# Kernel tuning notes

Measured on AMD Instinct MI355X. Metric: run time of the kernel, lower is better.

## Reference

```python
import jax, jax.numpy as jnp
import numpy as np

MAX_DISP = 48
N, C, H, W = 4, 32, 256, 512

def setup_inputs() -> dict:
    key = jax.random.key(0)
    k1, k2 = jax.random.split(key)
    l_fmap = jax.random.normal(k1, (N, C, H, W), dtype=jnp.float32)
    r_fmap = jax.random.normal(k2, (N, C, H, W), dtype=jnp.float32)
    return {"l_fmap": l_fmap, "r_fmap": r_fmap, "use_naive": 1}

def _cost_volume(l_fmap, r_fmap):
    # cost[n, d, h, w] = mean_c l[n,c,h,w] * r[n,c,h,w-d], zero where w < d
    n, c, h, w = l_fmap.shape
    items = []
    for d in range(MAX_DISP):
        if d == 0:
            r_shift = r_fmap
        else:
            # shift right by d with zero padding on the left (columns w<d -> 0)
            r_shift = jnp.pad(r_fmap[..., : w - d], ((0, 0), (0, 0), (0, 0), (d, 0)))
        items.append(jnp.mean(l_fmap * r_shift, axis=1))  # [n, h, w]
    return jnp.stack(items, axis=1)  # [n, max_disp, h, w]

def reference(l_fmap, r_fmap, use_naive):
    # naive and conv2d paths compute identical math; use_naive is ignored
    return _cost_volume(l_fmap, r_fmap)
```

## Files before the change

### kernel.cpp

```cpp
#include <hip/hip_runtime.h>

#define CC 32
#define HH 256
#define WW 512
#define NN 4
#define MAXD 48

#define WT 256
#define RW (WT + MAXD)
#define DTILE 8
#define WTILE 4
#define NT 384

__global__ __launch_bounds__(NT, 6)
void cost_volume_kernel(const float* __restrict__ L,
                        const float* __restrict__ R,
                        float* __restrict__ out)
{
    __shared__ float r_s[CC][RW];

    const int t  = threadIdx.x;
    const int w0 = blockIdx.x * WT;
    const int h  = blockIdx.y;
    const int n  = blockIdx.z;

    const size_t chw  = (size_t)HH * WW;
    const size_t rowB = (size_t)n * CC * chw + (size_t)h * WW;

    #pragma unroll
    for (int k = 0; k < 7; ++k) {
        int idx = t + NT * k;
        if (idx < 2432) {
            int c   = idx / 76;
            int j4  = idx - c * 76;
            int g   = w0 - MAXD + 4 * j4;
            float4 v = make_float4(0.f, 0.f, 0.f, 0.f);
            if (g >= 0)
                v = *(const float4*)(R + rowB + (size_t)c * chw + g);
            *(float4*)&r_s[c][4 * j4] = v;
        }
    }
    __syncthreads();

    const int wg = t & 63;
    const int dg = t >> 6;
    const int wb = wg * WTILE;
    const int d0 = dg * DTILE;
    const int jA = wb + 40 - d0;

    float acc[DTILE][WTILE];
    #pragma unroll
    for (int k = 0; k < DTILE; ++k)
        #pragma unroll
        for (int i = 0; i < WTILE; ++i)
            acc[k][i] = 0.f;

    const float* lp = L + rowB + w0 + wb;
    float4 lv0 = *(const float4*)(lp);
    float4 lv1 = *(const float4*)(lp + chw);
    for (int c = 0; c < CC; ++c) {
        float4 lnext;
        if (c + 2 < CC)
            lnext = *(const float4*)(lp + (size_t)(c + 2) * chw);
        float rv[12];
        #pragma unroll
        for (int q = 0; q < 3; ++q)
            *(float4*)&rv[4 * q] = *(const float4*)&r_s[c][jA + 4 * q];
        #pragma unroll
        for (int k = 0; k < DTILE; ++k) {
            acc[k][0] += lv0.x * rv[8 - k];
            acc[k][1] += lv0.y * rv[9 - k];
            acc[k][2] += lv0.z * rv[10 - k];
            acc[k][3] += lv0.w * rv[11 - k];
        }
        lv0 = lv1;
        lv1 = lnext;
    }

    const float inv = 1.0f / 32.0f;
    #pragma unroll
    for (int k = 0; k < DTILE; ++k) {
        const int d = d0 + k;
        float4 o = make_float4(acc[k][0] * inv, acc[k][1] * inv,
                               acc[k][2] * inv, acc[k][3] * inv);
        *(float4*)(out + (((size_t)n * MAXD + d) * HH + h) * WW + w0 + wb) = o;
    }
}

extern "C" void kernel_launch(void* const* d_in, const int* in_sizes, int n_in,
                              void* d_out, int out_size, void* d_ws, size_t ws_size,
                              hipStream_t stream) {
    const float* L = (const float*)d_in[0];
    const float* R = (const float*)d_in[1];
    float* out = (float*)d_out;
    dim3 grid(WW / WT, HH, NN);
    cost_volume_kernel<<<grid, dim3(NT, 1, 1), 0, stream>>>(L, R, out);
}
```

Baseline: 230.2 us.

## Stage L in shared memory and load R in two channel halves

Before, every thread read L straight from global memory with a two-deep register prefetch, so each L row was fetched six times, once per disparity group. Now the block loads L once into shared memory, cooperatively and coalesced, and every disparity group reads it from there. R is staged in two halves of 16 channels to keep the shared-memory footprint about the same. The cost is an extra barrier and a serialized load phase with no overlap of R loading and compute.

```diff
diff --git a/kernel.cpp b/kernel.cpp
--- a/kernel.cpp
+++ b/kernel.cpp
@@ -8,6 +8,7 @@
 
 #define WT 256
 #define RW (WT + MAXD)
+#define CH 16
 #define DTILE 8
 #define WTILE 4
 #define NT 384
@@ -17,7 +18,8 @@
                         const float* __restrict__ R,
                         float* __restrict__ out)
 {
-    __shared__ float r_s[CC][RW];
+    __shared__ float l_s[CC][WT];
+    __shared__ float r_s[CH][RW];
 
     const int t  = threadIdx.x;
     const int w0 = blockIdx.x * WT;
@@ -26,21 +28,6 @@
 
     const size_t chw  = (size_t)HH * WW;
     const size_t rowB = (size_t)n * CC * chw + (size_t)h * WW;
-
-    #pragma unroll
-    for (int k = 0; k < 7; ++k) {
-        int idx = t + NT * k;
-        if (idx < 2432) {
-            int c   = idx / 76;
-            int j4  = idx - c * 76;
-            int g   = w0 - MAXD + 4 * j4;
-            float4 v = make_float4(0.f, 0.f, 0.f, 0.f);
-            if (g >= 0)
-                v = *(const float4*)(R + rowB + (size_t)c * chw + g);
-            *(float4*)&r_s[c][4 * j4] = v;
-        }
-    }
-    __syncthreads();
 
     const int wg = t & 63;
     const int dg = t >> 6;
@@ -55,26 +42,53 @@
         for (int i = 0; i < WTILE; ++i)
             acc[k][i] = 0.f;
 
-    const float* lp = L + rowB + w0 + wb;
-    float4 lv0 = *(const float4*)(lp);
-    float4 lv1 = *(const float4*)(lp + chw);
-    for (int c = 0; c < CC; ++c) {
-        float4 lnext;
-        if (c + 2 < CC)
-            lnext = *(const float4*)(lp + (size_t)(c + 2) * chw);
-        float rv[12];
+    #pragma unroll
+    for (int k = 0; k < 6; ++k) {
+        int idx = t + NT * k;
+        if (idx < CC * 64) {
+            int c  = idx >> 6;
+            int j4 = idx & 63;
+            *(float4*)&l_s[c][4 * j4] =
+                *(const float4*)(L + rowB + (size_t)c * chw + w0 + 4 * j4);
+        }
+    }
+
+    for (int half = 0; half < 2; ++half) {
+        const int c0 = half * CH;
+        if (half) __syncthreads();
+
         #pragma unroll
-        for (int q = 0; q < 3; ++q)
-            *(float4*)&rv[4 * q] = *(const float4*)&r_s[c][jA + 4 * q];
-        #pragma unroll
-        for (int k = 0; k < DTILE; ++k) {
-            acc[k][0] += lv0.x * rv[8 - k];
-            acc[k][1] += lv0.y * rv[9 - k];
-            acc[k][2] += lv0.z * rv[10 - k];
-            acc[k][3] += lv0.w * rv[11 - k];
+        for (int k = 0; k < 4; ++k) {
+            int idx = t + NT * k;
+            if (idx < CH * 76) {
+                int c   = idx / 76;
+                int j4  = idx - c * 76;
+                int g   = w0 - MAXD + 4 * j4;
+                float4 v = make_float4(0.f, 0.f, 0.f, 0.f);
+                if (g >= 0)
+                    v = *(const float4*)(R + rowB + (size_t)(c0 + c) * chw + g);
+                *(float4*)&r_s[c][4 * j4] = v;
+            }
         }
-        lv0 = lv1;
-        lv1 = lnext;
+        __syncthreads();
+
+        #pragma unroll 4
+        for (int cc = 0; cc < CH; ++cc) {
+            const int c = c0 + cc;
+            float lf[4];
+            *(float4*)lf = *(const float4*)&l_s[c][wb];
+            float rv[12];
+            #pragma unroll
+            for (int q = 0; q < 3; ++q)
+                *(float4*)&rv[4 * q] = *(const float4*)&r_s[cc][jA + 4 * q];
+            #pragma unroll
+            for (int k = 0; k < DTILE; ++k) {
+                acc[k][0] += lf[0] * rv[8 - k];
+                acc[k][1] += lf[1] * rv[9 - k];
+                acc[k][2] += lf[2] * rv[10 - k];
+                acc[k][3] += lf[3] * rv[11 - k];
+            }
+        }
     }
 
     const float inv = 1.0f / 32.0f;
```

Result: slower. 253.5 us (+10.1%).

## Stage right feature map in two channel halves via async global-to-LDS loads

Applied to the files above, without the earlier changes.

The shared tile of the right feature map is split into two 16-channel halves. Each half is loaded with direct global-to-LDS loads (`__builtin_amdgcn_global_load_lds`), so the data no longer passes through registers. The second half is issued after the first barrier, letting its load overlap with compute on the first half, and a second barrier separates the two halves. Left-border zero padding is now written explicitly for the first width tile, and the channel loops are partially unrolled. The risk is that the extra barrier and the compiler's waitcnt placement limit how much overlap the hardware actually gets.

```diff
diff --git a/kernel.cpp b/kernel.cpp
--- a/kernel.cpp
+++ b/kernel.cpp
@@ -8,6 +8,7 @@
 
 #define WT 256
 #define RW (WT + MAXD)
+#define CH 16
 #define DTILE 8
 #define WTILE 4
 #define NT 384
@@ -17,7 +18,7 @@
                         const float* __restrict__ R,
                         float* __restrict__ out)
 {
-    __shared__ float r_s[CC][RW];
+    __shared__ float r_s[2][CH][RW];
 
     const int t  = threadIdx.x;
     const int w0 = blockIdx.x * WT;
@@ -27,26 +28,52 @@
     const size_t chw  = (size_t)HH * WW;
     const size_t rowB = (size_t)n * CC * chw + (size_t)h * WW;
 
-    #pragma unroll
-    for (int k = 0; k < 7; ++k) {
-        int idx = t + NT * k;
-        if (idx < 2432) {
-            int c   = idx / 76;
-            int j4  = idx - c * 76;
-            int g   = w0 - MAXD + 4 * j4;
-            float4 v = make_float4(0.f, 0.f, 0.f, 0.f);
-            if (g >= 0)
-                v = *(const float4*)(R + rowB + (size_t)c * chw + g);
-            *(float4*)&r_s[c][4 * j4] = v;
-        }
+    const int lane = t & 63;
+    const int wid  = t >> 6;
+    const int wb   = lane * WTILE;
+    const int d0   = wid * DTILE;
+    const int jA = wb + 40 - d0;
+
+#define ISSUE_HALF(half) do {                                                 \
+        _Pragma("unroll")                                                     \
+        for (int k = 0; k < 4; ++k) {                                         \
+            const int slot0 = k * NT + wid * 64;            \
+            if (slot0 < CH * 76) {                        \
+                const int idx = slot0 + lane;                                 \
+                const int c   = idx / 76;              \
+                const int j4  = idx - c * 76;                                 \
+                const int g   = w0 - MAXD + 4 * j4;             \
+                if (g >= 0) {                             \
+                    const float* gsrc =                                       \
+                        R + rowB + (size_t)((half) * CH + c) * chw + g;       \
+                    float* ldst = &r_s[0][0][0]                               \
+                                  + (size_t)(half) * (CH * RW) + 4 * slot0;   \
+                    __builtin_amdgcn_global_load_lds(                         \
+                        (const __attribute__((address_space(1))) void*)gsrc,  \
+                        (__attribute__((address_space(3))) void*)ldst,        \
+                        16, 0, 0);                                            \
+                }                                                             \
+            }                                                                 \
+        }                                                                     \
+    } while (0)
+
+    if (w0 == 0) {
+        int b  = t / 192;
+        int r2 = t - b * 192;
+        int c  = r2 / 12;
+        int j4 = r2 - c * 12;
+        *(float4*)&r_s[b][c][4 * j4] = make_float4(0.f, 0.f, 0.f, 0.f);
     }
+
+    const float* lp = L + rowB + w0 + wb;
+    float4 lv0 = *(const float4*)(lp);
+    float4 lv1 = *(const float4*)(lp + chw);
+
+    ISSUE_HALF(0);
+
     __syncthreads();
 
-    const int wg = t & 63;
-    const int dg = t >> 6;
-    const int wb = wg * WTILE;
-    const int d0 = dg * DTILE;
-    const int jA = wb + 40 - d0;
+    ISSUE_HALF(1);
 
     float acc[DTILE][WTILE];
     #pragma unroll
@@ -55,17 +82,13 @@
         for (int i = 0; i < WTILE; ++i)
             acc[k][i] = 0.f;
 
-    const float* lp = L + rowB + w0 + wb;
-    float4 lv0 = *(const float4*)(lp);
-    float4 lv1 = *(const float4*)(lp + chw);
-    for (int c = 0; c < CC; ++c) {
-        float4 lnext;
-        if (c + 2 < CC)
-            lnext = *(const float4*)(lp + (size_t)(c + 2) * chw);
+    #pragma unroll 4
+    for (int c = 0; c < CH; ++c) {
+        float4 lnext = *(const float4*)(lp + (size_t)(c + 2) * chw);
         float rv[12];
         #pragma unroll
         for (int q = 0; q < 3; ++q)
-            *(float4*)&rv[4 * q] = *(const float4*)&r_s[c][jA + 4 * q];
+            *(float4*)&rv[4 * q] = *(const float4*)&r_s[0][c][jA + 4 * q];
         #pragma unroll
         for (int k = 0; k < DTILE; ++k) {
             acc[k][0] += lv0.x * rv[8 - k];
@@ -76,6 +99,31 @@
         lv0 = lv1;
         lv1 = lnext;
     }
+
+    __syncthreads();
+
+    #pragma unroll 4
+    for (int cc = 0; cc < CH; ++cc) {
+        const int c = CH + cc;
+        float4 lnext;
+        if (c + 2 < CC)
+            lnext = *(const float4*)(lp + (size_t)(c + 2) * chw);
+        float rv[12];
+        #pragma unroll
+        for (int q = 0; q < 3; ++q)
+            *(float4*)&rv[4 * q] = *(const float4*)&r_s[1][cc][jA + 4 * q];
+        #pragma unroll
+        for (int k = 0; k < DTILE; ++k) {
+            acc[k][0] += lv0.x * rv[8 - k];
+            acc[k][1] += lv0.y * rv[9 - k];
+            acc[k][2] += lv0.z * rv[10 - k];
+            acc[k][3] += lv0.w * rv[11 - k];
+        }
+        lv0 = lv1;
+        lv1 = lnext;
+    }
+
+#undef ISSUE_HALF
 
     const float inv = 1.0f / 32.0f;
     #pragma unroll
```

Result: slower. 317.3 us (+37.8%).
